# Kernel tuning notes

Measured on AMD Instinct MI355X. Metric: run time of the kernel, lower is better.

The kernel has to match this reference:

```python
import jax, jax.numpy as jnp
import numpy as np

EPS_LOG = 2.220446049250313e-16  # np.finfo(float).eps used in ES_EE.ee
K = 2  # use_experts (top-k)


def _balance(v):
    v = v.astype(jnp.float32)
    # torch .var() is unbiased (ddof=1)
    return jnp.var(v, ddof=1) / (jnp.mean(v) ** 2 + 1e-10)


def setup_inputs() -> dict:
    key = jax.random.key(0)
    ks = jax.random.split(key, 8)
    B, C, H, W, E, D, HF = 2, 128, 128, 128, 6, 6, 512
    s = 0.02  # small init so exp(expert_out) stays in range
    return {
        "x": jax.random.normal(ks[0], (B, C, H, W), jnp.float32),
        "prompt": jax.random.normal(ks[1], (B, C), jnp.float32),
        "de_cls": jax.random.uniform(ks[2], (B, D), jnp.float32),
        "w_g": jax.random.normal(ks[3], (2 * C, E), jnp.float32) * s,
        "gate_boost": jnp.asarray(0.5, jnp.float32),
        "degra_w": jax.random.normal(ks[4], (D, E), jnp.float32) * s,
        "degra_b": jnp.zeros((E,), jnp.float32),
        "fc1_w": jax.random.normal(ks[5], (E, C, HF), jnp.float32) * s,
        "fc1_b": jnp.zeros((E, HF), jnp.float32),
        "fc2_w": jax.random.normal(ks[6], (E, HF, C), jnp.float32) * s,
        "fc2_b": jnp.zeros((E, C), jnp.float32),
    }


def reference(x, prompt, de_cls, w_g, gate_boost, degra_w, degra_b,
              fc1_w, fc1_b, fc2_w, fc2_b):
    # eval-mode forward (self.training == False -> no gating noise)
    B, C, H, W = x.shape
    N = B * H * W
    xf = jnp.transpose(x, (0, 2, 3, 1)).reshape(N, C)           # (b h w) c
    pf = jnp.broadcast_to(prompt[:, None, None, :], (B, H, W, C)).reshape(N, C)
    D = de_cls.shape[1]
    df = jnp.broadcast_to(de_cls[:, None, None, :], (B, H, W, D)).reshape(N, D)

    x_p = jnp.concatenate([xf, pf], axis=1)                     # [N, 2C]
    expert_bias = df @ degra_w + degra_b                        # degra_proj
    logits = x_p @ w_g + gate_boost * expert_bias               # [N, E]

    top_v, top_i = jax.lax.top_k(logits, K)
    gates_k = jax.nn.softmax(top_v, axis=1)                     # [N, K]
    w = jnp.zeros_like(logits).at[jnp.arange(N)[:, None], top_i].set(gates_k)

    Weight = w.sum(0)                                           # [E]
    s_load = (w > 0).sum(0).astype(jnp.float32)                 # w_load
    loss = _balance(Weight) + _balance(s_load)

    # per-expert Mlp on all tokens (w==0 rows contribute nothing to combine,
    # mathematically identical to the gather/scatter dispatch in ES_EE)
    hid = jax.nn.gelu(jnp.einsum('nc,ech->neh', xf, fc1_w) + fc1_b,
                      approximate=False)                        # [N, E, HF]
    out = jnp.einsum('neh,ehc->nec', hid, fc2_w) + fc2_b        # [N, E, C]

    # ES_EE.ee: log( sum_e gate_e * exp(out_e) ), zeros -> eps
    comb = jnp.einsum('ne,nec->nc', w, jnp.exp(out))
    comb = jnp.where(comb == 0, EPS_LOG, comb)
    y = jnp.log(comb)

    y = y.reshape(B, H, W, C).transpose(0, 3, 1, 2)             # b c h w
    return y, loss
```

## Files before the change

kernel.cpp:

```cpp
#include <hip/hip_runtime.h>
#include <math.h>

#define HW    16384
#define NTOK  32768
#define CDIM  128
#define HFDIM 512
#define NEXP  6

typedef __attribute__((ext_vector_type(8))) short short8;
typedef __attribute__((ext_vector_type(8))) unsigned short ushort8v;
typedef __attribute__((ext_vector_type(16))) float f32x16;
typedef unsigned long long u64;

#define OFF_XFB    0UL
#define OFF_LIST   8388608UL
#define OFF_GATES  9175040UL
#define OFF_OUTBUF 9437184UL
#define OFF_WT1    42991616UL
#define OFF_WT2    43778048UL
#define OFF_BIAS   44564480UL
#define OFF_CNT    44564736UL
#define OFF_WSUM   44564992UL

__device__ __forceinline__ unsigned int bf16_1(float f) {
    unsigned int u = __float_as_uint(f);
    return (u + 0x7FFFu + ((u >> 16) & 1)) >> 16;
}
__device__ __forceinline__ unsigned int bf16pair(float lo, float hi) {
    return bf16_1(lo) | (bf16_1(hi) << 16);
}
__device__ __forceinline__ float gelu_f(float v) {
    return __fdividef(v, 1.0f + __expf(-1.702f * v));
}

#define GLDS16(src, dst) __builtin_amdgcn_global_load_lds( \
    (const __attribute__((address_space(1))) void*)(src),  \
    (__attribute__((address_space(3))) void*)(dst), 16, 0, 0)

__device__ __forceinline__ f32x16 MFMA_B(short8 a, short8 b, f32x16 c) {
    return __builtin_amdgcn_mfma_f32_32x32x16_bf16(a, b, c, 0, 0, 0);
}

__global__ __launch_bounds__(64) void prep_kernel(
    const float* __restrict__ prompt, const float* __restrict__ de_cls,
    const float* __restrict__ w_g, const float* __restrict__ gate_boost,
    const float* __restrict__ degra_w, const float* __restrict__ degra_b,
    float* __restrict__ bias, int* __restrict__ cnt, float* __restrict__ wsum)
{
    int t = threadIdx.x;
    if (t < 2 * NEXP) {
        int b = t / NEXP, e = t % NEXP;
        float acc = 0.f;
        for (int c = 0; c < CDIM; ++c)
            acc = fmaf(prompt[b*CDIM + c], w_g[(CDIM + c)*NEXP + e], acc);
        float db = 0.f;
        for (int d = 0; d < 6; ++d)
            db = fmaf(de_cls[b*6 + d], degra_w[d*NEXP + e], db);
        bias[b*NEXP + e] = acc + gate_boost[0] * (db + degra_b[e]);
    }
    if (t >= 32 && t < 32 + NEXP) cnt[t - 32] = 0;
    if (t >= 40 && t < 40 + NEXP) wsum[t - 40] = 0.f;
}

__global__ __launch_bounds__(256) void wconv_kernel(
    const float* __restrict__ fc1_w, const float* __restrict__ fc2_w,
    unsigned short* __restrict__ wt1, unsigned short* __restrict__ wt2)
{
    __shared__ unsigned short ls[128][128];
    const int bid = blockIdx.x;
    const int e = bid >> 3, which = (bid >> 2) & 1, ch = bid & 3;
    const int t = threadIdx.x;
    #pragma unroll 4
    for (int i = 0; i < 16; ++i) {
        int id = t + 256 * i;
        int k = id >> 5, q = id & 31;
        const float* p = which
            ? (fc2_w + (size_t)e*65536 + (size_t)(ch*128 + k)*128 + q*4)
            : (fc1_w + (size_t)e*65536 + (size_t)k*512 + ch*128 + q*4);
        float4 v = *(const float4*)p;
        u64 pk = (u64)bf16_1(v.x) | ((u64)bf16_1(v.y) << 16)
               | ((u64)bf16_1(v.z) << 32) | ((u64)bf16_1(v.w) << 48);
        *(u64*)&ls[k][q*4] = pk;
    }
    __syncthreads();
    #pragma unroll 2
    for (int i = 0; i < 8; ++i) {
        int id = t + 256 * i;
        int col = id & 127, kg = id >> 7;
        unsigned short v[8];
        #pragma unroll
        for (int j = 0; j < 8; ++j) v[j] = ls[kg*8 + j][col];
        int4 pk;
        pk.x = v[0] | (v[1] << 16); pk.y = v[2] | (v[3] << 16);
        pk.z = v[4] | (v[5] << 16); pk.w = v[6] | (v[7] << 16);
        if (which) {
            int h = kg >> 3, ks8 = kg & 7;
            *(int4*)(wt2 + (((size_t)(e*8 + ch*2 + h)) << 13)
                     + (size_t)col*64 + (((ks8 ^ (col & 7)) & 7) << 3)) = pk;
        } else {
            *(int4*)(wt1 + (((size_t)(e*4 + ch)) << 14)
                     + (size_t)col*128 + (((kg ^ (col & 15)) & 15) << 3)) = pk;
        }
    }
}

__global__ __launch_bounds__(256) void gate_kernel(
    const float* __restrict__ x, const float* __restrict__ w_g,
    const float* __restrict__ bias, unsigned short* __restrict__ xfb,
    int* __restrict__ list, float* __restrict__ gates,
    int* __restrict__ cnt, float* __restrict__ wsum)
{
    __shared__ float xs[CDIM][65];
    __shared__ float wgs[CDIM][NEXP];
    __shared__ int   cnt_s[NEXP];
    __shared__ float ws_s[NEXP];
    __shared__ int   base_s[NEXP];
    const int t = threadIdx.x;
    const int n0 = blockIdx.x * 64;
    const int b = n0 >> 14;
    const int hw0 = n0 & (HW - 1);

    for (int i = t; i < CDIM * NEXP; i += 256) wgs[i / NEXP][i % NEXP] = w_g[i];
    if (t < NEXP) { cnt_s[t] = 0; ws_s[t] = 0.f; }

    const float* xb = x + (size_t)b * CDIM * HW + hw0;
    #pragma unroll 4
    for (int i = 0; i < 32; ++i) {
        int idx = t + 256 * i;
        int c = idx >> 6, j = idx & 63;
        xs[c][j] = xb[(size_t)c * HW + j];
    }
    __syncthreads();
    unsigned int* xo = (unsigned int*)xfb;
    #pragma unroll 4
    for (int i = 0; i < 16; ++i) {
        int idx = t + 256 * i;
        int tk = idx >> 6, cp = idx & 63;
        xo[(size_t)(n0 + tk) * 64 + cp] = bf16pair(xs[2*cp][tk], xs[2*cp+1][tk]);
    }

    int i0 = 0, i1 = 0, s0 = 0, s1 = 0;
    float g0 = 0.f, g1 = 0.f;
    if (t < 64) {
        float lg[NEXP];
        #pragma unroll
        for (int e = 0; e < NEXP; ++e) lg[e] = bias[b*NEXP + e];
        for (int c = 0; c < CDIM; ++c) {
            float xv = xs[c][t];
            #pragma unroll
            for (int e = 0; e < NEXP; ++e) lg[e] = fmaf(xv, wgs[c][e], lg[e]);
        }
        i0 = 0;
        #pragma unroll
        for (int e = 1; e < NEXP; ++e) if (lg[e] > lg[i0]) i0 = e;
        i1 = (i0 == 0) ? 1 : 0;
        #pragma unroll
        for (int e = 0; e < NEXP; ++e) if (e != i0 && lg[e] > lg[i1]) i1 = e;
        float e1 = expf(lg[i1] - lg[i0]);
        g0 = 1.f / (1.f + e1);
        g1 = e1 * g0;
        s0 = atomicAdd(&cnt_s[i0], 1);
        s1 = atomicAdd(&cnt_s[i1], 1);
        atomicAdd(&ws_s[i0], g0);
        atomicAdd(&ws_s[i1], g1);
    }
    __syncthreads();
    if (t < NEXP) {
        base_s[t] = atomicAdd(&cnt[t], cnt_s[t]);
        atomicAdd(&wsum[t], ws_s[t]);
    }
    __syncthreads();
    if (t < 64) {
        int n = n0 + t;
        list[i0 * NTOK + base_s[i0] + s0] = 2 * n;
        list[i1 * NTOK + base_s[i1] + s1] = 2 * n + 1;
        gates[2 * n]     = g0;
        gates[2 * n + 1] = g1;
    }
}

__global__ void loss_kernel(const int* __restrict__ cnt,
                            const float* __restrict__ wsum,
                            float* __restrict__ out_loss)
{
    if (threadIdx.x == 0 && blockIdx.x == 0) {
        float mw = 0.f, mc = 0.f;
        for (int e = 0; e < NEXP; ++e) { mw += wsum[e]; mc += (float)cnt[e]; }
        mw /= NEXP; mc /= NEXP;
        float vw = 0.f, vc = 0.f;
        for (int e = 0; e < NEXP; ++e) {
            float dw = wsum[e] - mw, dc = (float)cnt[e] - mc;
            vw += dw * dw; vc += dc * dc;
        }
        vw /= (NEXP - 1); vc /= (NEXP - 1);
        out_loss[0] = vw / (mw * mw + 1e-10f) + vc / (mc * mc + 1e-10f);
    }
}

__global__ __launch_bounds__(256, 4) void expert_kernel(
    const unsigned short* __restrict__ xfb, const int* __restrict__ list,
    const int* __restrict__ cnt, const float* __restrict__ gates,
    const unsigned short* __restrict__ wt1, const unsigned short* __restrict__ wt2,
    const float* __restrict__ fc1_b, const float* __restrict__ fc2_b,
    unsigned short* __restrict__ outbuf)
{
    __shared__ unsigned short w1c[8192];
    __shared__ unsigned short w2c[8192];
    __shared__ unsigned short hs[4096];
    const int e = blockIdx.x;
    const int ne = cnt[e];
    const int base = blockIdx.y * 64;
    if (base >= ne) return;
    const int t = threadIdx.x;
    const int w = t >> 6, l = t & 63;
    const int l31 = l & 31, lk = (l >> 5) * 8;
    const int th = (w & 1) * 32;
    const int hfh = w >> 1;

    int r = base + l;
    int a = (r < ne) ? list[e*NTOK + r] : -1;
    float g = (a >= 0) ? gates[a] : 0.f;
    int tok = (a >= 0) ? (a >> 1) : 0;

    short8 afr[8];
    {
        int tokv = __shfl(tok, th + l31);
        const unsigned short* xr = xfb + (size_t)tokv*128 + lk;
        #pragma unroll
        for (int ks = 0; ks < 8; ++ks)
            afr[ks] = *(const short8*)(xr + ks*16);
    }

    f32x16 zz;
    #pragma unroll
    for (int i = 0; i < 16; ++i) zz[i] = 0.0f;
    f32x16 oacc0 = zz, oacc1 = zz;

    for (int j = 0; j < 8; ++j) {
        {
            const unsigned short* s1 = wt1 + (((size_t)(e*4 + (j >> 1))) << 14)
                                     + (j & 1)*8192 + (w*4)*512 + l*8;
            const unsigned short* s2 = wt2 + (((size_t)(e*8 + j)) << 13)
                                     + (w*4)*512 + l*8;
            #pragma unroll
            for (int i = 0; i < 4; ++i)
                GLDS16(s1 + i*512, &w1c[(w*4 + i)*512]);
            #pragma unroll
            for (int i = 0; i < 4; ++i)
                GLDS16(s2 + i*512, &w2c[(w*4 + i)*512]);
        }
        __syncthreads();
        f32x16 acc1 = zz;
        {
            int brow = hfh*32 + l31;
            #pragma unroll
            for (int ks = 0; ks < 8; ++ks) {
                int k = ks*16 + lk;
                short8 bfr = *(const short8*)((const char*)w1c + brow*256
                             + ((((k >> 3) ^ brow) & 15) << 4));
                acc1 = MFMA_B(afr[ks], bfr, acc1);
            }
        }
        {
            int col = hfh*32 + l31;
            float b1 = fc1_b[(size_t)e*HFDIM + j*64 + col];
            #pragma unroll
            for (int rr = 0; rr < 16; ++rr) {
                float h = gelu_f(acc1[rr] + b1);
                int row = th + (rr & 3) + 8*(rr >> 2) + 4*(l >> 5);
                *(unsigned short*)((char*)hs + row*128
                    + ((((col >> 3) ^ (row & 7)) & 7) << 4) + ((col & 7) << 1))
                    = (unsigned short)bf16_1(h);
            }
        }
        __syncthreads();
        {
            int arow = th + l31;
            #pragma unroll
            for (int ks = 0; ks < 4; ++ks) {
                int k = ks*16 + lk;
                short8 a2 = *(const short8*)((const char*)hs + arow*128
                             + ((((k >> 3) ^ (arow & 7)) & 7) << 4));
                int crow0 = hfh*64 + l31;
                int crow1 = hfh*64 + 32 + l31;
                short8 b20 = *(const short8*)((const char*)w2c + crow0*128
                             + ((((k >> 3) ^ (crow0 & 7)) & 7) << 4));
                short8 b21 = *(const short8*)((const char*)w2c + crow1*128
                             + ((((k >> 3) ^ (crow1 & 7)) & 7) << 4));
                oacc0 = MFMA_B(a2, b20, oacc0);
                oacc1 = MFMA_B(a2, b21, oacc1);
            }
        }
        __syncthreads();
    }

    float b20 = fc2_b[(size_t)e*CDIM + hfh*64 + l31];
    float b21 = fc2_b[(size_t)e*CDIM + hfh*64 + 32 + l31];
    #pragma unroll
    for (int rr = 0; rr < 16; ++rr) {
        int crow = (rr & 3) + 8*(rr >> 2) + 4*(l >> 5);
        int rloc = th + crow;
        int av   = __shfl(a, rloc);
        float gv = __shfl(g, rloc);
        if (av < 0) continue;
        unsigned short* po = outbuf + (size_t)av*CDIM + hfh*64 + l31;
        po[0]  = (unsigned short)bf16_1(gv * __expf(oacc0[rr] + b20));
        po[32] = (unsigned short)bf16_1(gv * __expf(oacc1[rr] + b21));
    }
}

__global__ __launch_bounds__(256) void combine_kernel(
    const unsigned short* __restrict__ outbuf, float* __restrict__ out)
{
    __shared__ float ys[64][129];
    const int t = threadIdx.x;
    const int n0 = blockIdx.x * 64;
    const int b = n0 >> 14;
    const int hw0 = n0 & (HW - 1);
    #pragma unroll
    for (int i = 0; i < 4; ++i) {
        int idx = t + 256 * i;
        int tk = idx >> 4, c8 = (idx & 15) * 8;
        const unsigned short* p = outbuf + (size_t)(n0 + tk) * 256 + c8;
        ushort8v p0 = *(const ushort8v*)p;
        ushort8v p1 = *(const ushort8v*)(p + 128);
        const float EPSL = 2.2204460492503131e-16f;
        #pragma unroll
        for (int j = 0; j < 8; ++j) {
            float v = __uint_as_float((unsigned)p0[j] << 16)
                    + __uint_as_float((unsigned)p1[j] << 16);
            ys[tk][c8 + j] = __logf(v == 0.f ? EPSL : v);
        }
    }
    __syncthreads();
    float* ob = out + (size_t)b * CDIM * HW + hw0;
    #pragma unroll 4
    for (int i = 0; i < 32; ++i) {
        int idx = t + 256 * i;
        int c = idx >> 6;
        int j = idx & 63;
        ob[(size_t)c * HW + j] = ys[j][c];
    }
}

extern "C" void kernel_launch(void* const* d_in, const int* in_sizes, int n_in,
                              void* d_out, int out_size, void* d_ws, size_t ws_size,
                              hipStream_t stream)
{
    const float* x       = (const float*)d_in[0];
    const float* prompt  = (const float*)d_in[1];
    const float* de_cls  = (const float*)d_in[2];
    const float* w_g     = (const float*)d_in[3];
    const float* gboost  = (const float*)d_in[4];
    const float* degra_w = (const float*)d_in[5];
    const float* degra_b = (const float*)d_in[6];
    const float* fc1_w   = (const float*)d_in[7];
    const float* fc1_b   = (const float*)d_in[8];
    const float* fc2_w   = (const float*)d_in[9];
    const float* fc2_b   = (const float*)d_in[10];
    float* out = (float*)d_out;
    char* ws = (char*)d_ws;

    unsigned short* xfb  = (unsigned short*)(ws + OFF_XFB);
    int*   list   = (int*)(ws + OFF_LIST);
    float* gates  = (float*)(ws + OFF_GATES);
    unsigned short* outbuf = (unsigned short*)(ws + OFF_OUTBUF);
    unsigned short* wt1 = (unsigned short*)(ws + OFF_WT1);
    unsigned short* wt2 = (unsigned short*)(ws + OFF_WT2);
    float* bias   = (float*)(ws + OFF_BIAS);
    int*   cnt    = (int*)(ws + OFF_CNT);
    float* wsum   = (float*)(ws + OFF_WSUM);

    prep_kernel<<<1, 64, 0, stream>>>(prompt, de_cls, w_g, gboost, degra_w,
                                      degra_b, bias, cnt, wsum);
    wconv_kernel<<<48, 256, 0, stream>>>(fc1_w, fc2_w, wt1, wt2);
    gate_kernel<<<512, 256, 0, stream>>>(x, w_g, bias, xfb, list, gates, cnt, wsum);
    loss_kernel<<<1, 64, 0, stream>>>(cnt, wsum, out + (size_t)NTOK * CDIM);
    dim3 eg(NEXP, 512);
    expert_kernel<<<eg, 256, 0, stream>>>(xfb, list, cnt, gates, wt1, wt2,
                                          fc1_b, fc2_b, outbuf);
    combine_kernel<<<512, 256, 0, stream>>>(outbuf, out);
}
```

Measured before the change: 103.7 us.

## Keep expert hidden activations in registers and widen expert tile to 128 tokens

```diff
diff --git a/kernel.cpp b/kernel.cpp
--- a/kernel.cpp
+++ b/kernel.cpp
@@ -31,6 +31,11 @@
 }
 __device__ __forceinline__ float gelu_f(float v) {
     return __fdividef(v, 1.0f + __expf(-1.702f * v));
+}
+__device__ __forceinline__ short8 mk8(unsigned a, unsigned b, unsigned c, unsigned d) {
+    union { unsigned u[4]; short8 s; } x;
+    x.u[0] = a; x.u[1] = b; x.u[2] = c; x.u[3] = d;
+    return x.s;
 }
 
 #define GLDS16(src, dst) __builtin_amdgcn_global_load_lds( \
@@ -83,6 +88,7 @@
         *(u64*)&ls[k][q*4] = pk;
     }
     __syncthreads();
+    unsigned short* dst = (which ? wt2 : wt1) + (((size_t)(e*4 + ch)) << 14);
     #pragma unroll 2
     for (int i = 0; i < 8; ++i) {
         int id = t + 256 * i;
@@ -93,14 +99,7 @@
         int4 pk;
         pk.x = v[0] | (v[1] << 16); pk.y = v[2] | (v[3] << 16);
         pk.z = v[4] | (v[5] << 16); pk.w = v[6] | (v[7] << 16);
-        if (which) {
-            int h = kg >> 3, ks8 = kg & 7;
-            *(int4*)(wt2 + (((size_t)(e*8 + ch*2 + h)) << 13)
-                     + (size_t)col*64 + (((ks8 ^ (col & 7)) & 7) << 3)) = pk;
-        } else {
-            *(int4*)(wt1 + (((size_t)(e*4 + ch)) << 14)
-                     + (size_t)col*128 + (((kg ^ (col & 15)) & 15) << 3)) = pk;
-        }
+        *(int4*)(dst + (size_t)col*128 + (((kg ^ (col & 15)) & 15) << 3)) = pk;
     }
 }
 
@@ -197,35 +196,32 @@
     }
 }
 
-__global__ __launch_bounds__(256, 4) void expert_kernel(
+__global__ __launch_bounds__(256, 2) void expert_kernel(
     const unsigned short* __restrict__ xfb, const int* __restrict__ list,
     const int* __restrict__ cnt, const float* __restrict__ gates,
     const unsigned short* __restrict__ wt1, const unsigned short* __restrict__ wt2,
     const float* __restrict__ fc1_b, const float* __restrict__ fc2_b,
     unsigned short* __restrict__ outbuf)
 {
-    __shared__ unsigned short w1c[8192];
-    __shared__ unsigned short w2c[8192];
-    __shared__ unsigned short hs[4096];
+    __shared__ unsigned short w1c[16384];
+    __shared__ unsigned short w2c[16384];
     const int e = blockIdx.x;
     const int ne = cnt[e];
-    const int base = blockIdx.y * 64;
+    const int base = blockIdx.y * 128;
     if (base >= ne) return;
     const int t = threadIdx.x;
     const int w = t >> 6, l = t & 63;
     const int l31 = l & 31, lk = (l >> 5) * 8;
-    const int th = (w & 1) * 32;
-    const int hfh = w >> 1;
-
-    int r = base + l;
+    const bool islo = (l < 32);
+
+    int r = base + w*32 + l31;
     int a = (r < ne) ? list[e*NTOK + r] : -1;
     float g = (a >= 0) ? gates[a] : 0.f;
     int tok = (a >= 0) ? (a >> 1) : 0;
 
     short8 afr[8];
     {
-        int tokv = __shfl(tok, th + l31);
-        const unsigned short* xr = xfb + (size_t)tokv*128 + lk;
+        const unsigned short* xr = xfb + (size_t)tok*128 + lk;
         #pragma unroll
         for (int ks = 0; ks < 8; ++ks)
             afr[ks] = *(const short8*)(xr + ks*16);
@@ -234,78 +230,83 @@
     f32x16 zz;
     #pragma unroll
     for (int i = 0; i < 16; ++i) zz[i] = 0.0f;
-    f32x16 oacc0 = zz, oacc1 = zz;
-
-    for (int j = 0; j < 8; ++j) {
+    f32x16 oacc[4] = {zz, zz, zz, zz};
+
+    for (int gp = 0; gp < 4; ++gp) {
         {
-            const unsigned short* s1 = wt1 + (((size_t)(e*4 + (j >> 1))) << 14)
-                                     + (j & 1)*8192 + (w*4)*512 + l*8;
-            const unsigned short* s2 = wt2 + (((size_t)(e*8 + j)) << 13)
-                                     + (w*4)*512 + l*8;
-            #pragma unroll
-            for (int i = 0; i < 4; ++i)
-                GLDS16(s1 + i*512, &w1c[(w*4 + i)*512]);
-            #pragma unroll
-            for (int i = 0; i < 4; ++i)
-                GLDS16(s2 + i*512, &w2c[(w*4 + i)*512]);
+            const unsigned short* s1 = wt1 + (((size_t)(e*4 + gp)) << 14) + w*4096 + l*8;
+            const unsigned short* s2 = wt2 + (((size_t)(e*4 + gp)) << 14) + w*4096 + l*8;
+            #pragma unroll
+            for (int i = 0; i < 8; ++i)
+                GLDS16(s1 + i*512, &w1c[w*4096 + i*512]);
+            #pragma unroll
+            for (int i = 0; i < 8; ++i)
+                GLDS16(s2 + i*512, &w2c[w*4096 + i*512]);
         }
         __syncthreads();
-        f32x16 acc1 = zz;
-        {
-            int brow = hfh*32 + l31;
+
+        short8 pa[8];
+        #pragma unroll
+        for (int ch = 0; ch < 4; ++ch) {
+            f32x16 c1 = zz;
+            int arow = ch*32 + l31;
             #pragma unroll
             for (int ks = 0; ks < 8; ++ks) {
                 int k = ks*16 + lk;
-                short8 bfr = *(const short8*)((const char*)w1c + brow*256
-                             + ((((k >> 3) ^ brow) & 15) << 4));
-                acc1 = MFMA_B(afr[ks], bfr, acc1);
+                short8 wf = *(const short8*)((const char*)w1c + arow*256
+                             + ((((k >> 3) ^ (arow & 15)) & 15) << 4));
+                c1 = MFMA_B(wf, afr[ks], c1);
             }
-        }
-        {
-            int col = hfh*32 + l31;
-            float b1 = fc1_b[(size_t)e*HFDIM + j*64 + col];
-            #pragma unroll
-            for (int rr = 0; rr < 16; ++rr) {
-                float h = gelu_f(acc1[rr] + b1);
-                int row = th + (rr & 3) + 8*(rr >> 2) + 4*(l >> 5);
-                *(unsigned short*)((char*)hs + row*128
-                    + ((((col >> 3) ^ (row & 7)) & 7) << 4) + ((col & 7) << 1))
-                    = (unsigned short)bf16_1(h);
+            const float* bb = fc1_b + (size_t)e*HFDIM + gp*128 + ch*32 + 4*(l >> 5);
+            float4 b0 = *(const float4*)(bb);
+            float4 b1 = *(const float4*)(bb + 8);
+            float4 b2 = *(const float4*)(bb + 16);
+            float4 b3 = *(const float4*)(bb + 24);
+            float bias[16] = {b0.x, b0.y, b0.z, b0.w, b1.x, b1.y, b1.z, b1.w,
+                              b2.x, b2.y, b2.z, b2.w, b3.x, b3.y, b3.z, b3.w};
+            unsigned int pr[8];
+            #pragma unroll
+            for (int i = 0; i < 8; ++i) {
+                float h0 = gelu_f(c1[2*i]     + bias[2*i]);
+                float h1 = gelu_f(c1[2*i + 1] + bias[2*i + 1]);
+                pr[i] = bf16pair(h0, h1);
             }
+            unsigned int rx0 = __shfl_xor(islo ? pr[2] : pr[0], 32);
+            unsigned int rx1 = __shfl_xor(islo ? pr[3] : pr[1], 32);
+            unsigned int rx2 = __shfl_xor(islo ? pr[6] : pr[4], 32);
+            unsigned int rx3 = __shfl_xor(islo ? pr[7] : pr[5], 32);
+            pa[2*ch]     = mk8(islo ? pr[0] : rx0, islo ? pr[1] : rx1,
+                               islo ? rx0 : pr[2], islo ? rx1 : pr[3]);
+            pa[2*ch + 1] = mk8(islo ? pr[4] : rx2, islo ? pr[5] : rx3,
+                               islo ? rx2 : pr[6], islo ? rx3 : pr[7]);
+        }
+        #pragma unroll
+        for (int kg = 0; kg < 8; ++kg) {
+            #pragma unroll
+            for (int ct = 0; ct < 4; ++ct) {
+                int crow = ct*32 + l31;
+                short8 bf = *(const short8*)((const char*)w2c + crow*256
+                             + ((((kg*2 + (l >> 5)) ^ (crow & 15)) & 15) << 4));
+                oacc[ct] = MFMA_B(pa[kg], bf, oacc[ct]);
+            }
         }
         __syncthreads();
-        {
-            int arow = th + l31;
-            #pragma unroll
-            for (int ks = 0; ks < 4; ++ks) {
-                int k = ks*16 + lk;
-                short8 a2 = *(const short8*)((const char*)hs + arow*128
-                             + ((((k >> 3) ^ (arow & 7)) & 7) << 4));
-                int crow0 = hfh*64 + l31;
-                int crow1 = hfh*64 + 32 + l31;
-                short8 b20 = *(const short8*)((const char*)w2c + crow0*128
-                             + ((((k >> 3) ^ (crow0 & 7)) & 7) << 4));
-                short8 b21 = *(const short8*)((const char*)w2c + crow1*128
-                             + ((((k >> 3) ^ (crow1 & 7)) & 7) << 4));
-                oacc0 = MFMA_B(a2, b20, oacc0);
-                oacc1 = MFMA_B(a2, b21, oacc1);
-            }
-        }
-        __syncthreads();
-    }
-
-    float b20 = fc2_b[(size_t)e*CDIM + hfh*64 + l31];
-    float b21 = fc2_b[(size_t)e*CDIM + hfh*64 + 32 + l31];
+    }
+
+    float bc[4];
+    #pragma unroll
+    for (int ct = 0; ct < 4; ++ct)
+        bc[ct] = fc2_b[(size_t)e*CDIM + ct*32 + l31];
     #pragma unroll
     for (int rr = 0; rr < 16; ++rr) {
         int crow = (rr & 3) + 8*(rr >> 2) + 4*(l >> 5);
-        int rloc = th + crow;
-        int av   = __shfl(a, rloc);
-        float gv = __shfl(g, rloc);
+        int av   = __shfl(a, crow);
+        float gv = __shfl(g, crow);
         if (av < 0) continue;
-        unsigned short* po = outbuf + (size_t)av*CDIM + hfh*64 + l31;
-        po[0]  = (unsigned short)bf16_1(gv * __expf(oacc0[rr] + b20));
-        po[32] = (unsigned short)bf16_1(gv * __expf(oacc1[rr] + b21));
+        unsigned short* po = outbuf + (size_t)av*CDIM + l31;
+        #pragma unroll
+        for (int ct = 0; ct < 4; ++ct)
+            po[ct*32] = (unsigned short)bf16_1(gv * __expf(oacc[ct][rr] + bc[ct]));
     }
 }
 
@@ -376,7 +377,7 @@
     wconv_kernel<<<48, 256, 0, stream>>>(fc1_w, fc2_w, wt1, wt2);
     gate_kernel<<<512, 256, 0, stream>>>(x, w_g, bias, xfb, list, gates, cnt, wsum);
     loss_kernel<<<1, 64, 0, stream>>>(cnt, wsum, out + (size_t)NTOK * CDIM);
-    dim3 eg(NEXP, 512);
+    dim3 eg(NEXP, 256);
     expert_kernel<<<eg, 256, 0, stream>>>(xfb, list, cnt, gates, wt1, wt2,
                                           fc1_b, fc2_b, outbuf);
     combine_kernel<<<512, 256, 0, stream>>>(outbuf, out);
```

Measured after the change: 125.1 us. 20.7% more time.
